# Optimization experiments

Measured on AMD Instinct MI355X. Metric: run time of the kernel, lower is better.

Reference implementation:

```python
import jax, jax.numpy as jnp
import numpy as np

# NOTE on reconstructed deps (not shown in source):
#  - utils.mmnorm(x): max-magnitude norm, x / (max|x| over last dim + eps)
#  - model.LearnableFourierResampler(din, dout, nf): x -> Linear(din,nf) -> [sin,cos] -> Linear(2nf,dout)
#  - utils.pscan(q, fn, identity): Hillis-Steele log-depth scan: for n in 1,2,4,...:
#        q = fn(x=q, y=shift_right(q, n, fill=identity))   (Scanner.forward(x, y) cats (y, x))

B, T, C, NF = 8, 2048, 1024, 64
EPS = 1e-6

def mmnorm(x):
    return x / (jnp.max(jnp.abs(x), axis=-1, keepdims=True) + EPS)

def setup_inputs() -> dict:
    key = jax.random.key(0)
    ks = jax.random.split(key, 8)
    def w(k, shape, fan_in):
        return jax.random.normal(k, shape, jnp.float32) * (1.0 / np.sqrt(fan_in))
    return {
        "x": jax.random.normal(ks[0], (B, T, C), jnp.float32),
        "attn_W": w(ks[1], (C, 2 * C), C),
        "attn_b": jnp.zeros((2 * C,), jnp.float32),
        "freq_W": w(ks[2], (2 * C, NF), 2 * C),
        "freq_b": jnp.zeros((NF,), jnp.float32),
        "out_W": w(ks[3], (2 * NF, C), 2 * NF),
        "out_b": jnp.zeros((C,), jnp.float32),
        "proj_W": w(ks[4], (C, C), C),
        "proj_b": jnp.zeros((C,), jnp.float32),
        "identity": jax.random.uniform(ks[5], (C,), jnp.float32),
    }

def _scanner(y, x, freq_W, freq_b, out_W, out_b):
    # Scanner.forward(x, y): z = cat((y, x)); Fourier resample; mmnorm
    z = jnp.concatenate([y, x], axis=-1)                      # [B,T,2C]
    f = z @ freq_W + freq_b                                   # [B,T,NF]
    z = jnp.concatenate([jnp.sin(f), jnp.cos(f)], -1) @ out_W + out_b  # [B,T,C]
    return mmnorm(z)

def reference(x, attn_W, attn_b, freq_W, freq_b, out_W, out_b, proj_W, proj_b, identity):
    b, t, c = x.shape
    qv = x @ attn_W + attn_b
    q, v = qv[..., :c], qv[..., c:]
    # Hillis-Steele parallel scan with nonlinear learned combine
    n = 1
    while n < t:
        prev = jnp.concatenate(
            [jnp.broadcast_to(identity, (b, n, c)), q[:, : t - n]], axis=1)
        q = _scanner(prev, q, freq_W, freq_b, out_W, out_b)
        n *= 2
    Y = q * v
    return Y @ proj_W + proj_b
```

## Files before the change

kernel.cpp:

```cpp
#include <hip/hip_runtime.h>
#include <hip/hip_bf16.h>
#include <math.h>


#define R_ROWS 16384
#define T_DIM  2048
#define C_DIM  1024

typedef unsigned short u16;
typedef __attribute__((ext_vector_type(8))) short short8;
typedef __attribute__((ext_vector_type(4))) float f32x4;

__device__ __forceinline__ u16 f2bf(float f) {
  union { float f; unsigned u; } v; v.f = f;
  unsigned r = v.u + 0x7fffu + ((v.u >> 16) & 1u);
  return (u16)(r >> 16);
}
__device__ __forceinline__ float bf2f(u16 h) {
  union { unsigned u; float f; } v; v.u = ((unsigned)h) << 16;
  return v.f;
}
__device__ __forceinline__ void gld16(const void* g, void* l) {
  __builtin_amdgcn_global_load_lds(
      (const __attribute__((address_space(1))) void*)g,
      (__attribute__((address_space(3))) void*)l, 16, 0, 0);
}

__device__ __forceinline__ void cvtT_tile(const float* W, u16* Wt, int K, int N,
                                          int noff, int k0, int n0,
                                          float (*t)[33]) {
  const int tx = threadIdx.x & 31, ty = threadIdx.x >> 5;
#pragma unroll
  for (int i = 0; i < 32; i += 8)
    t[ty + i][tx] = W[(size_t)(k0 + ty + i) * N + noff + n0 + tx];
  __syncthreads();
#pragma unroll
  for (int i = 0; i < 32; i += 8)
    Wt[(size_t)(n0 + ty + i) * K + k0 + tx] = f2bf(t[tx][ty + i]);
}

__global__ __launch_bounds__(256) void prep_weights(
    const float* __restrict__ x, const float* __restrict__ attn_W,
    const float* __restrict__ proj_W, const float* __restrict__ out_W,
    const float* __restrict__ freq_W, u16* __restrict__ Xb,
    u16* __restrict__ aWt, u16* __restrict__ pWt, u16* __restrict__ w2t,
    u16* __restrict__ w1f, u16* __restrict__ Wqb, u16* __restrict__ Wob) {
  __shared__ float t[32][33];
  const int bid = blockIdx.x;
  if (bid < 8192) {
    const int i = bid * 256 + threadIdx.x;
    const float4 a = ((const float4*)x)[2 * i];
    const float4 b = ((const float4*)x)[2 * i + 1];
    alignas(16) u16 tt[8] = {f2bf(a.x), f2bf(a.y), f2bf(a.z), f2bf(a.w),
                             f2bf(b.x), f2bf(b.y), f2bf(b.z), f2bf(b.w)};
    ((uint4*)Xb)[i] = *(const uint4*)tt;
  } else if (bid < 9216) {
    const int b = bid - 8192;
    cvtT_tile(attn_W, aWt, 1024, 2048, 1024, (b & 31) * 32, (b >> 5) * 32, t);
  } else if (bid < 10240) {
    const int b = bid - 9216;
    cvtT_tile(proj_W, pWt, 1024, 1024, 0, (b & 31) * 32, (b >> 5) * 32, t);
  } else if (bid < 10368) {
    const int b = bid - 10240;
    cvtT_tile(out_W, w2t, 128, 1024, 0, (b & 3) * 32, (b >> 2) * 32, t);
  } else if (bid < 10496) {
    const int b = bid - 10368;
    const int k0 = (b & 63) * 32, n0 = (b >> 6) * 32;
    const int tx = threadIdx.x & 31, ty = threadIdx.x >> 5;
#pragma unroll
    for (int i = 0; i < 32; i += 8)
      t[ty + i][tx] = freq_W[(size_t)(k0 + ty + i) * 64 + n0 + tx];
    __syncthreads();
#pragma unroll
    for (int i = 0; i < 32; i += 8) {
      const int k = k0 + tx;
      const int row = (n0 + ty + i) + ((k >= 1024) ? 64 : 0);
      w1f[(size_t)row * 1024 + (k & 1023)] = f2bf(t[tx][ty + i]);
    }
  } else if (bid < 11520) {
    const int c = bid - 10496, k0 = threadIdx.x * 4;
    const float4 a = *(const float4*)&attn_W[(size_t)c * 2048 + k0];
    alignas(8) u16 tt[4] = {f2bf(a.x), f2bf(a.y), f2bf(a.z), f2bf(a.w)};
    *(uint2*)&Wqb[(size_t)c * 1024 + k0] = *(const uint2*)tt;
  } else {
    const int c = bid - 11520, k0 = threadIdx.x * 4;
    const float4 a = *(const float4*)&out_W[(size_t)c * 1024 + k0];
    alignas(8) u16 tt[4] = {f2bf(a.x), f2bf(a.y), f2bf(a.z), f2bf(a.w)};
    *(uint2*)&Wob[(size_t)c * 1024 + k0] = *(const uint2*)tt;
  }
}

__device__ __forceinline__ void gm_body(const u16* w1f, const u16* B,
                                        u16* Mt, int ldO, int n0, u16* As) {
  const int tid = threadIdx.x, lane = tid & 63, w = tid >> 6;
  const int ln = lane & 15, qd = lane >> 4;
  const int wm = w & 1, wn = w >> 1;
  const int srow = w * 32 + (lane >> 3);
  const int scol = ((lane & 7) ^ ((lane >> 3) & 7)) * 8;
  f32x4 acc[4][2] = {};
  for (int kt = 0; kt < 1024; kt += 64) {
    __syncthreads();
#pragma unroll
    for (int j = 0; j < 4; j++)
      gld16(&w1f[(size_t)(srow + j * 8) * 1024 + kt + scol],
            &As[(w * 32 + j * 8) * 64]);
    __syncthreads();
#pragma unroll
    for (int ks = 0; ks < 2; ks++) {
      short8 af[4];
#pragma unroll
      for (int i = 0; i < 4; i++) {
        const int ar = wm * 64 + i * 16 + ln;
        af[i] = *(const short8*)&As[ar * 64 + ((ks * 4 + qd) ^ (ar & 7)) * 8];
      }
#pragma unroll
      for (int nt = 0; nt < 2; nt++) {
        const short8 b = *(const short8*)&B[(size_t)(n0 + wn * 32 + nt * 16 + ln) * 1024 +
                                            kt + ks * 32 + qd * 8];
#pragma unroll
        for (int i = 0; i < 4; i++)
          acc[i][nt] = __builtin_amdgcn_mfma_f32_16x16x32_bf16(af[i], b, acc[i][nt], 0, 0, 0);
      }
    }
  }
#pragma unroll
  for (int i = 0; i < 4; i++)
#pragma unroll
    for (int nt = 0; nt < 2; nt++)
#pragma unroll
      for (int r = 0; r < 4; r++)
        Mt[(size_t)(wm * 64 + i * 16 + qd * 4 + r) * ldO +
           n0 + wn * 32 + nt * 16 + ln] = f2bf(acc[i][nt][r]);
}

__device__ __forceinline__ void dotred_body(const float* ab, const u16* w1f,
                                            float* outv, float* red) {
  const int tid = threadIdx.x, j = tid >> 1, part = tid & 1;
  float s = 0.f;
  for (int k = part * 512; k < part * 512 + 512; k++)
    s += ab[k] * bf2f(w1f[(size_t)j * 1024 + k]);
  red[tid] = s;
  __syncthreads();
  if (part == 0) outv[j] = red[2 * j] + red[2 * j + 1];
}

__global__ __launch_bounds__(256) void prep_small(
    const float* __restrict__ ident, const float* __restrict__ freq_W,
    const float* __restrict__ attn_b, const float* __restrict__ out_b,
    const u16* __restrict__ w1f, const u16* __restrict__ Wqb,
    const u16* __restrict__ Wob, float* __restrict__ fid,
    float* __restrict__ bgv, float* __restrict__ c1,
    u16* __restrict__ Mt, u16* __restrict__ W21t) {
  __shared__ u16 sh[8192];
  float* red = (float*)sh;
  const int bid = blockIdx.x;
  if (bid == 0) {
    const int tid = threadIdx.x;
    const int j = tid >> 2, part = tid & 3;
    float s = 0.f;
    for (int k = part * 256; k < part * 256 + 256; k++)
      s += ident[k] * freq_W[(size_t)k * 64 + j];
    red[tid] = s;
    __syncthreads();
    if (part == 0) fid[j] = red[tid] + red[tid + 1] + red[tid + 2] + red[tid + 3];
  } else if (bid == 1) {
    dotred_body(attn_b, w1f, bgv, red);
  } else if (bid == 2) {
    dotred_body(out_b, w1f, c1, red);
  } else if (bid < 19) {
    gm_body(w1f, Wqb, Mt, 1024, (bid - 3) * 64, sh);
  } else {
    gm_body(w1f, Wob, W21t, 128, (bid - 19) * 64, sh);
  }
}

#define GEMM_KLOOP(Aptr, Bptr)                                                 \
  const int tid = threadIdx.x, lane = tid & 63, w = tid >> 6;                  \
  const int ln = lane & 15, qd = lane >> 4;                                    \
  const int wm = w & 1, wn = w >> 1;                                           \
  const int nbx = gridDim.x;                                                   \
  const int bid0 = blockIdx.y * nbx + blockIdx.x;                              \
  const int nwg = nbx * gridDim.y;                                             \
  const int bid = (bid0 & 7) * (nwg >> 3) + (bid0 >> 3);                       \
  const int n0 = (bid % nbx) * 128, m0 = (bid / nbx) * 128;                    \
  const int srow = w * 32 + (lane >> 3);                                       \
  const int sl = (lane & 7) ^ ((lane >> 3) & 7);                               \
  const int scol = sl * 8;                                                     \
  f32x4 acc[4][4] = {};                                                        \
  for (int kt = 0; kt < 1024; kt += 64) {                                      \
    __syncthreads();                                                           \
    _Pragma("unroll") for (int j = 0; j < 4; j++) {                            \
      gld16(&Aptr[(size_t)(m0 + srow + j * 8) * 1024 + kt + scol],             \
            &As[(w * 32 + j * 8) * 64]);                                       \
      gld16(&Bptr[(size_t)(n0 + srow + j * 8) * 1024 + kt + scol],             \
            &Bs[(w * 32 + j * 8) * 64]);                                       \
    }                                                                          \
    __syncthreads();                                                           \
    _Pragma("unroll") for (int ks = 0; ks < 2; ks++) {                         \
      short8 af[4], bf_[4];                                                    \
      _Pragma("unroll") for (int i = 0; i < 4; i++) {                          \
        const int ar = wm * 64 + i * 16 + ln;                                  \
        af[i] = *(const short8*)&As[ar * 64 + ((ks * 4 + qd) ^ (ar & 7)) * 8]; \
      }                                                                        \
      _Pragma("unroll") for (int j = 0; j < 4; j++) {                          \
        const int br = wn * 64 + j * 16 + ln;                                  \
        bf_[j] = *(const short8*)&Bs[br * 64 + ((ks * 4 + qd) ^ (br & 7)) * 8];\
      }                                                                        \
      _Pragma("unroll") for (int i = 0; i < 4; i++)                            \
      _Pragma("unroll") for (int j = 0; j < 4; j++)                            \
        acc[i][j] = __builtin_amdgcn_mfma_f32_16x16x32_bf16(af[i], bf_[j],     \
                                                            acc[i][j], 0, 0, 0);\
    }                                                                          \
  }                                                                            \
  __syncthreads();

__global__ __launch_bounds__(256) void gemm_vg_mfma(
    const u16* __restrict__ A, const u16* __restrict__ Bt,
    const float* __restrict__ bias, const float* __restrict__ bg,
    u16* __restrict__ Vb, float* __restrict__ G) {
  __shared__ u16 S[16384];
  u16* As = S;
  u16* Bs = S + 8192;
  GEMM_KLOOP(A, Bt)
  if (n0 < 1024) {
#pragma unroll
    for (int j = 0; j < 4; j++) {
      const int col = wn * 64 + j * 16 + ln;
      const float bv = bias[n0 + col];
#pragma unroll
      for (int i = 0; i < 4; i++)
#pragma unroll
        for (int r = 0; r < 4; r++)
          S[(wm * 64 + i * 16 + qd * 4 + r) * 128 + col] = f2bf(acc[i][j][r] + bv);
    }
    __syncthreads();
#pragma unroll
    for (int it = 0; it < 8; it++) {
      const int idx = it * 256 + tid;
      const int row = idx >> 4, seg = idx & 15;
      *(uint4*)&Vb[(size_t)(m0 + row) * 1024 + n0 + seg * 8] = ((const uint4*)S)[idx];
    }
  } else {
#pragma unroll
    for (int j = 0; j < 4; j++) {
      const int col = wn * 64 + j * 16 + ln;
      const float bv = bg[col];
#pragma unroll
      for (int i = 0; i < 4; i++)
#pragma unroll
        for (int r = 0; r < 4; r++)
          G[(size_t)(m0 + wm * 64 + i * 16 + qd * 4 + r) * 128 + col] =
              acc[i][j][r] + bv;
    }
  }
}

__global__ __launch_bounds__(256) void gemm_proj_mfma(
    const u16* __restrict__ A, const u16* __restrict__ Bt,
    const float* __restrict__ bias, float* __restrict__ OUT) {
  __shared__ u16 S[16384];
  u16* As = S;
  u16* Bs = S + 8192;
  GEMM_KLOOP(A, Bt)
  float* Csf = (float*)S;
#pragma unroll
  for (int p = 0; p < 2; p++) {
    if (wm == p) {
#pragma unroll
      for (int j = 0; j < 4; j++) {
        const int col = wn * 64 + j * 16 + ln;
        const float bv = bias[n0 + col];
#pragma unroll
        for (int i = 0; i < 4; i++)
#pragma unroll
          for (int r = 0; r < 4; r++)
            Csf[(i * 16 + qd * 4 + r) * 128 + col] = acc[i][j][r] + bv;
      }
    }
    __syncthreads();
#pragma unroll
    for (int it = 0; it < 8; it++) {
      const int idx = it * 256 + tid;
      const int row = idx >> 5, seg = idx & 31;
      *(uint4*)&OUT[(size_t)(m0 + p * 64 + row) * 1024 + n0 + seg * 4] =
          ((const uint4*)Csf)[idx];
    }
    __syncthreads();
  }
}

__global__ __launch_bounds__(1024, 4) void scan_fused(
    const float* __restrict__ Gsrc, float* __restrict__ Gdst,
    const u16* __restrict__ W21t, const u16* __restrict__ W2t,
    const float* __restrict__ b1, const float* __restrict__ b2,
    const float* __restrict__ fid, const float* __restrict__ c1,
    const u16* __restrict__ Vb, u16* __restrict__ Yout, int n, int flags) {
  __shared__ u16 S[64 * 128];
  __shared__ unsigned rmax[64];
  const int tid = threadIdx.x, lane = tid & 63, wv = tid >> 6;
  const int ln = lane & 15, qd = lane >> 4;
  const int bid = blockIdx.x;
  const int r0 = (((bid & 7) << 5) + (bid >> 3)) * 64;
  if (tid < 64) rmax[tid] = 0u;
  {
    const int r = tid >> 4, js = (tid & 15) << 2;
    const int gr = r0 + r, tl = gr & (T_DIM - 1);
    const float* g1p = (tl >= n) ? &Gsrc[(size_t)(gr - n) * 128 + js] : &fid[js];
    const float4 g1 = *(const float4*)g1p;
    const float4 g2 = *(const float4*)&Gsrc[(size_t)gr * 128 + 64 + js];
    const float4 bb = *(const float4*)&b1[js];
    float f[4] = {g1.x + g2.x + bb.x, g1.y + g2.y + bb.y,
                  g1.z + g2.z + bb.z, g1.w + g2.w + bb.w};
    alignas(8) u16 sn[4], cs[4];
#pragma unroll
    for (int c = 0; c < 4; c++) {
      float sv, cv;
      __sincosf(f[c], &sv, &cv);
      sn[c] = f2bf(sv);
      cs[c] = f2bf(cv);
    }
    const int u = js >> 3, half = (js >> 2) & 1, rx = r & 7;
    const int ps = (u ^ rx) & 7;
    const int pc = 8 | ps;
    *(uint2*)&S[r * 128 + ps * 8 + half * 4] = *(const uint2*)sn;
    *(uint2*)&S[r * 128 + pc * 8 + half * 4] = *(const uint2*)cs;
  }
  __syncthreads();
  const u16* w2b = W2t + (size_t)wv * 64 * 128;
  f32x4 acc[4][4] = {};
#pragma unroll
  for (int ks = 0; ks < 4; ks++) {
    short8 af[4];
#pragma unroll
    for (int i = 0; i < 4; i++) {
      const int ar = i * 16 + ln;
      const int u = ks * 4 + qd;
      af[i] = *(const short8*)&S[ar * 128 + ((u & 8) | ((u ^ ar) & 7)) * 8];
    }
#pragma unroll
    for (int nt = 0; nt < 4; nt++) {
      const short8 b = *(const short8*)&w2b[(size_t)(nt * 16 + ln) * 128 + ks * 32 + qd * 8];
#pragma unroll
      for (int i = 0; i < 4; i++)
        acc[i][nt] = __builtin_amdgcn_mfma_f32_16x16x32_bf16(b, af[i], acc[i][nt], 0, 0, 0);
    }
  }
  float mx[4] = {0.f, 0.f, 0.f, 0.f};
#pragma unroll
  for (int nt = 0; nt < 4; nt++) {
    const float4 bb = *(const float4*)&b2[wv * 64 + nt * 16 + qd * 4];
    const float br4[4] = {bb.x, bb.y, bb.z, bb.w};
#pragma unroll
    for (int i = 0; i < 4; i++)
#pragma unroll
      for (int r = 0; r < 4; r++) {
        const float v = acc[i][nt][r] + br4[r];
        acc[i][nt][r] = v;
        mx[i] = fmaxf(mx[i], fabsf(v));
      }
  }
#pragma unroll
  for (int i = 0; i < 4; i++) {
    float v = mx[i];
    v = fmaxf(v, __shfl_xor(v, 16, 64));
    v = fmaxf(v, __shfl_xor(v, 32, 64));
    if (lane < 16) atomicMax(&rmax[i * 16 + lane], __float_as_uint(v));
  }
  __syncthreads();
  if (flags & 1) {
    float inv[4];
#pragma unroll
    for (int i = 0; i < 4; i++)
      inv[i] = 1.0f / (__uint_as_float(rmax[i * 16 + ln]) + 1e-6f);
#pragma unroll
    for (int i = 0; i < 4; i++) {
      const int row = i * 16 + ln;
#pragma unroll
      for (int nt = 0; nt < 4; nt++) {
        const int col = wv * 64 + nt * 16 + qd * 4;
        const uint2 vv = *(const uint2*)&Vb[(size_t)(r0 + row) * 1024 + col];
        const u16* vp = (const u16*)&vv;
        uint2 pv;
        pv.x = (unsigned)f2bf(acc[i][nt][0] * inv[i] * bf2f(vp[0])) |
               ((unsigned)f2bf(acc[i][nt][1] * inv[i] * bf2f(vp[1])) << 16);
        pv.y = (unsigned)f2bf(acc[i][nt][2] * inv[i] * bf2f(vp[2])) |
               ((unsigned)f2bf(acc[i][nt][3] * inv[i] * bf2f(vp[3])) << 16);
        *(uint2*)&Yout[(size_t)(r0 + row) * 1024 + col] = pv;
      }
    }
  }
  if (flags & 2) {
    const int wm3 = wv & 3, wn3 = wv >> 2;
    f32x4 g[2] = {};
#pragma unroll
    for (int ks = 0; ks < 4; ks++) {
      const int ar = wm3 * 16 + ln;
      const int u = ks * 4 + qd;
      const short8 a = *(const short8*)&S[ar * 128 + ((u & 8) | ((u ^ ar) & 7)) * 8];
#pragma unroll
      for (int c = 0; c < 2; c++) {
        const short8 b = *(const short8*)&W21t[(size_t)(wn3 * 32 + c * 16 + ln) * 128 +
                                               ks * 32 + qd * 8];
        g[c] = __builtin_amdgcn_mfma_f32_16x16x32_bf16(a, b, g[c], 0, 0, 0);
      }
    }
#pragma unroll
    for (int c = 0; c < 2; c++) {
      const int col = wn3 * 32 + c * 16 + ln;
      const float cb = c1[col];
#pragma unroll
      for (int r = 0; r < 4; r++) {
        const int row = wm3 * 16 + qd * 4 + r;
        const float invr = 1.0f / (__uint_as_float(rmax[row]) + 1e-6f);
        Gdst[(size_t)(r0 + row) * 128 + col] = (g[c][r] + cb) * invr;
      }
    }
  }
}

extern "C" void kernel_launch(void* const* d_in, const int* in_sizes, int n_in,
                              void* d_out, int out_size, void* d_ws, size_t ws_size,
                              hipStream_t stream) {
  const float* x      = (const float*)d_in[0];
  const float* attn_W = (const float*)d_in[1];
  const float* attn_b = (const float*)d_in[2];
  const float* freq_W = (const float*)d_in[3];
  const float* freq_b = (const float*)d_in[4];
  const float* out_W  = (const float*)d_in[5];
  const float* out_b  = (const float*)d_in[6];
  const float* proj_W = (const float*)d_in[7];
  const float* proj_b = (const float*)d_in[8];
  const float* ident  = (const float*)d_in[9];
  float* out = (float*)d_out;

  const size_t RC = (size_t)R_ROWS * C_DIM;
  u16* Xb  = (u16*)d_ws;
  u16* Qb  = Xb + RC;
  u16* Wqb = Qb;
  u16* Wob = Qb + (size_t)1024 * 1024;
  u16* Vb  = Qb + RC;
  u16* aWt = Vb + RC;
  u16* Mt  = aWt + (size_t)1024 * 1024;
  u16* pWt = aWt + (size_t)2048 * 1024;
  u16* w2t = pWt + (size_t)1024 * 1024;
  u16* w1f = w2t + (size_t)1024 * 128;
  float* Ga  = (float*)(w1f + (size_t)128 * 1024);
  float* Gb  = Ga + (size_t)R_ROWS * 128;
  float* fid = Gb + (size_t)R_ROWS * 128;
  float* c1  = fid + 64;
  float* bgv = c1 + 128;
  u16* W21t  = (u16*)(bgv + 128);

  prep_weights<<<11648, 256, 0, stream>>>(x, attn_W, proj_W, out_W, freq_W,
                                          Xb, aWt, pWt, w2t, w1f, Wqb, Wob);
  prep_small<<<21, 256, 0, stream>>>(ident, freq_W, attn_b, out_b, w1f, Wqb,
                                     Wob, fid, bgv, c1, Mt, W21t);

  gemm_vg_mfma<<<dim3(9, 128), 256, 0, stream>>>(Xb, aWt, attn_b + 1024, bgv,
                                                 Vb, Ga);

  float* gs = Ga;
  float* gd = Gb;
  for (int n = 1; n < 1024; n <<= 1) {
    scan_fused<<<256, 1024, 0, stream>>>(gs, gd, W21t, w2t, freq_b, out_b, fid,
                                         c1, Vb, Xb, n, 2);
    float* t = gs; gs = gd; gd = t;
  }
  scan_fused<<<256, 1024, 0, stream>>>(gs, gd, W21t, w2t, freq_b, out_b, fid,
                                       c1, Vb, Xb, 1024, 1);

  gemm_proj_mfma<<<dim3(8, 128), 256, 0, stream>>>(Xb, pWt, proj_b, out);
}
```

Measured before the change: 356.9 us.

## Replace projection GEMM with 256x256 tiled double-buffered kernel

The final projection GEMM moves from a 128x128 tile with 256 threads to a 256x256 tile with 512 threads. Each wave now holds an 8x4 MFMA accumulator block, K is staged through two LDS buffers so the next tile loads while the current one computes, and block IDs are remapped across XCDs. The aim is more operand reuse per load and hidden global latency. In exchange it uses 128KB of shared memory, more registers per thread, and launches only 256 workgroups.

```diff
diff --git a/kernel.cpp b/kernel.cpp
--- a/kernel.cpp
+++ b/kernel.cpp
@@ -255,34 +255,89 @@
   }
 }
 
-__global__ __launch_bounds__(256) void gemm_proj_mfma(
+__global__ __launch_bounds__(512, 2) void gemm_proj2(
     const u16* __restrict__ A, const u16* __restrict__ Bt,
     const float* __restrict__ bias, float* __restrict__ OUT) {
-  __shared__ u16 S[16384];
-  u16* As = S;
-  u16* Bs = S + 8192;
-  GEMM_KLOOP(A, Bt)
-  float* Csf = (float*)S;
-#pragma unroll
-  for (int p = 0; p < 2; p++) {
-    if (wm == p) {
-#pragma unroll
-      for (int j = 0; j < 4; j++) {
-        const int col = wn * 64 + j * 16 + ln;
-        const float bv = bias[n0 + col];
-#pragma unroll
-        for (int i = 0; i < 4; i++)
+  __shared__ u16 A0[16384];
+  __shared__ u16 B0[16384];
+  __shared__ u16 A1[16384];
+  __shared__ u16 B1[16384];
+  const int tid = threadIdx.x, lane = tid & 63, wv = tid >> 6;
+  const int ln = lane & 15, qd = lane >> 4;
+  const int wm2 = wv >> 2, wn2 = wv & 3;
+  const int nbx = gridDim.x;
+  const int bid0 = blockIdx.y * nbx + blockIdx.x;
+  const int nwg = nbx * gridDim.y;
+  const int bid = (bid0 & 7) * (nwg >> 3) + (bid0 >> 3);
+  const int n0 = (bid % nbx) * 256, m0 = (bid / nbx) * 256;
+  const int srow = wv * 32 + (lane >> 3);
+  const int scol = ((lane & 7) ^ ((lane >> 3) & 7)) * 8;
+  f32x4 acc[8][4] = {};
+
+#define PSTAGE(kk, dA, dB)                                                     \
+  _Pragma("unroll") for (int j = 0; j < 4; j++) {                              \
+    gld16(&A[(size_t)(m0 + srow + j * 8) * 1024 + (kk) + scol],                \
+          &dA[(srow + j * 8) * 64]);                                           \
+    gld16(&Bt[(size_t)(n0 + srow + j * 8) * 1024 + (kk) + scol],               \
+          &dB[(srow + j * 8) * 64]);                                           \
+  }
+
+#define PCOMPUTE(sA, sB)                                                       \
+  _Pragma("unroll") for (int ks = 0; ks < 2; ks++) {                           \
+    short8 af[8], bf_[4];                                                      \
+    _Pragma("unroll") for (int i = 0; i < 8; i++) {                            \
+      const int ar = wm2 * 128 + i * 16 + ln;                                  \
+      af[i] = *(const short8*)&sA[ar * 64 + ((ks * 4 + qd) ^ (ar & 7)) * 8];   \
+    }                                                                          \
+    _Pragma("unroll") for (int j = 0; j < 4; j++) {                            \
+      const int br = wn2 * 64 + j * 16 + ln;                                   \
+      bf_[j] = *(const short8*)&sB[br * 64 + ((ks * 4 + qd) ^ (br & 7)) * 8];  \
+    }                                                                          \
+    _Pragma("unroll") for (int i = 0; i < 8; i++)                              \
+    _Pragma("unroll") for (int j = 0; j < 4; j++)                              \
+      acc[i][j] = __builtin_amdgcn_mfma_f32_16x16x32_bf16(af[i], bf_[j],       \
+                                                          acc[i][j], 0, 0, 0); \
+  }
+
+  PSTAGE(0, A0, B0)
+  __syncthreads();
+#pragma unroll 1
+  for (int kt = 0; kt < 16; kt += 2) {
+    PSTAGE((kt + 1) * 64, A1, B1)
+    PCOMPUTE(A0, B0)
+    __syncthreads();
+    if (kt + 2 < 16) {
+      PSTAGE((kt + 2) * 64, A0, B0)
+    }
+    PCOMPUTE(A1, B1)
+    __syncthreads();
+  }
+#undef PSTAGE
+#undef PCOMPUTE
+
+  float* Csf = (float*)A0;
+#pragma unroll 1
+  for (int p = 0; p < 8; p++) {
+    if (wm2 == (p >> 2)) {
+#pragma unroll
+      for (int ii = 0; ii < 2; ii++) {
+        const int i = (p & 3) * 2 + ii;
+#pragma unroll
+        for (int j = 0; j < 4; j++) {
+          const int col = wn2 * 64 + j * 16 + ln;
+          const float bv = bias[n0 + col];
 #pragma unroll
           for (int r = 0; r < 4; r++)
-            Csf[(i * 16 + qd * 4 + r) * 128 + col] = acc[i][j][r] + bv;
-      }
-    }
-    __syncthreads();
-#pragma unroll
-    for (int it = 0; it < 8; it++) {
-      const int idx = it * 256 + tid;
-      const int row = idx >> 5, seg = idx & 31;
-      *(uint4*)&OUT[(size_t)(m0 + p * 64 + row) * 1024 + n0 + seg * 4] =
+            Csf[(ii * 16 + qd * 4 + r) * 256 + col] = acc[i][j][r] + bv;
+        }
+      }
+    }
+    __syncthreads();
+#pragma unroll
+    for (int it = 0; it < 4; it++) {
+      const int idx = it * 512 + tid;
+      const int row = idx >> 6, seg = idx & 63;
+      *(uint4*)&OUT[(size_t)(m0 + p * 32 + row) * 1024 + n0 + seg * 4] =
           ((const uint4*)Csf)[idx];
     }
     __syncthreads();
@@ -469,5 +524,5 @@
   scan_fused<<<256, 1024, 0, stream>>>(gs, gd, W21t, w2t, freq_b, out_b, fid,
                                        c1, Vb, Xb, 1024, 1);
 
-  gemm_proj_mfma<<<dim3(8, 128), 256, 0, stream>>>(Xb, pWt, proj_b, out);
-}
+  gemm_proj2<<<dim3(4, 64), 512, 0, stream>>>(Xb, pWt, proj_b, out);
+}
```

Measured after the change: 937.9 us. 163% more time.
